# Performance work log

Measured on AMD Instinct MI355X. Metric: run time of the kernel, lower is better.

Reference implementation:

```python
import jax, jax.numpy as jnp
import numpy as np

# Static config (matches init_kwargs / link_info)
E = 8            # ep_size * num_local_experts
C = 1024         # expert capacity
D_IN = 4096      # in_features (d_ff)
D_OUT = 1024     # out_features (d_model)
B, S = 2, 2048   # inputs_shape = (B, S, D_OUT); tokens = B*S = 4096


def setup_inputs() -> dict:
    key = jax.random.key(0)
    ks = jax.random.split(key, 5)
    inputs = jax.random.normal(ks[0], (E * C + B * S, D_IN), dtype=jnp.float32)
    expert_w = jax.random.normal(ks[1], (E, D_IN, D_OUT), dtype=jnp.float32) * 0.02
    expert_b = jnp.zeros((E, D_OUT), dtype=jnp.float32)
    residual_w = jax.random.normal(ks[2], (D_IN, D_OUT), dtype=jnp.float32) * 0.02
    residual_b = jnp.zeros((D_OUT,), dtype=jnp.float32)
    combine_weights = jax.random.uniform(ks[3], (B * S, E, C), dtype=jnp.float32)
    residual_weight = jax.random.uniform(ks[4], (B, S, 2), dtype=jnp.float32)
    return {
        "inputs": inputs,
        "expert_w": expert_w,
        "expert_b": expert_b,
        "residual_w": residual_w,
        "residual_b": residual_b,
        "combine_weights": combine_weights,
        "residual_weight": residual_weight,
    }


def reference(inputs, expert_w, expert_b, residual_w, residual_b,
              combine_weights, residual_weight):
    # front_output: dispatched tokens [E, C, D_IN]
    front = inputs[: E * C].reshape(E, C, D_IN)
    # behind experts: per-expert second FFN linear -> [E, C, D_OUT]
    expert_out = jnp.einsum("ecd,edm->ecm", front, expert_w) + expert_b[:, None, :]
    # AllToAll over the expert-parallel group is identity for a single group.
    # combine: un-dispatch tokens, weighted scatter-gather 'sec,ecm->sm'
    combined = jnp.einsum("sec,ecm->sm", combine_weights, expert_out)
    output = combined.reshape(B, S, D_OUT)
    # residual MLP second linear on the tail slice of inputs
    resid_inter = inputs[E * C :].reshape(B, S, D_IN)
    resid_out = jnp.einsum("bsd,dm->bsm", resid_inter, residual_w) + residual_b
    # blend: output * w0 + residual * w1
    return output * residual_weight[..., 0:1] + resid_out * residual_weight[..., 1:]
```

## Files before the change

### kernel.cpp

```cpp
#include <hip/hip_runtime.h>
#include <hip/hip_bf16.h>

typedef __bf16 bf16_t;
typedef __bf16 bf16x8 __attribute__((ext_vector_type(8)));
typedef float f32x4 __attribute__((ext_vector_type(4)));

#define DEVI static __device__ __forceinline__

static constexpr int E_ = 8, C_ = 1024, DIN = 4096, DOUT = 1024, TOK = 4096;
static constexpr int BM = 128, BN = 128, BK = 64;
static constexpr int NT = 512;

static constexpr size_t WS_WT  = 0;
static constexpr size_t WS_RWT = WS_WT  + (size_t)E_ * DOUT * DIN * 2;
static constexpr size_t WS_EOT = WS_RWT + (size_t)DOUT * DIN * 2;

DEVI int swz(int row, int col) {
    return (col & ~63) | ((col & 56) ^ ((row & 7) << 3)) | (col & 7);
}

__global__ __launch_bounds__(256)
void transpose_cast_kernel(const float* __restrict__ expert_w,
                           const float* __restrict__ residual_w,
                           bf16_t* __restrict__ wt, bf16_t* __restrict__ rwt)
{
    __shared__ float tile[32][33];
    const int z = blockIdx.z;
    const float* src;
    bf16_t* dst;
    if (z < 8) { src = expert_w + (size_t)z * DIN * DOUT; dst = wt + (size_t)z * DOUT * DIN; }
    else       { src = residual_w;                         dst = rwt; }
    const int c0 = blockIdx.x * 32;
    const int r0 = blockIdx.y * 32;
    const int tx = threadIdx.x, ty = threadIdx.y;
#pragma unroll
    for (int k = 0; k < 4; ++k)
        tile[ty + 8 * k][tx] = src[(size_t)(r0 + ty + 8 * k) * DOUT + c0 + tx];
    __syncthreads();
#pragma unroll
    for (int k = 0; k < 4; ++k) {
        const int row = c0 + ty + 8 * k;
        const int col = r0 + tx;
        dst[(size_t)row * DIN + swz(row, col)] = (bf16_t)tile[tx][ty + 8 * k];
    }
}

template<int NELEM>
DEVI void stage_bf16(bf16_t* lds, const bf16_t* g, int ld, int tid)
{
    constexpr int PER_WAVE = NELEM / 8;
    constexpr int NI = PER_WAVE / 512;
    const int w = tid >> 6, l = tid & 63;
#pragma unroll
    for (int i = 0; i < NI; ++i) {
        const int eoff = w * PER_WAVE + i * 512 + l * 8;
        const int r = eoff >> 6, c = eoff & 63;
        const bf16_t* gp = g + (size_t)r * ld + c;
        bf16_t* lp = lds + w * PER_WAVE + i * 512;
        __builtin_amdgcn_global_load_lds(
            (const __attribute__((address_space(1))) void*)gp,
            (__attribute__((address_space(3))) void*)lp, 16, 0, 0);
    }
}

template<int NELEM>
DEVI void stage_f32(bf16_t* lds, const float* g, int ld, int tid)
{
    constexpr int NI = NELEM / (NT * 8);
#pragma unroll
    for (int i = 0; i < NI; ++i) {
        const int eoff = i * NT * 8 + tid * 8;
        const int r = eoff >> 6, c = eoff & 63;
        const float* gp = g + (size_t)r * ld + c;
        f32x4 v0 = *(const f32x4*)(gp);
        f32x4 v1 = *(const f32x4*)(gp + 4);
        bf16x8 h;
        h[0] = (bf16_t)v0[0]; h[1] = (bf16_t)v0[1];
        h[2] = (bf16_t)v0[2]; h[3] = (bf16_t)v0[3];
        h[4] = (bf16_t)v1[0]; h[5] = (bf16_t)v1[1];
        h[6] = (bf16_t)v1[2]; h[7] = (bf16_t)v1[3];
        const int cs = (c & 56) ^ ((r & 7) << 3);
        *(bf16x8*)(lds + r * 64 + cs) = h;
    }
}

__global__ __launch_bounds__(NT, 4)
void expert_gemm(const bf16_t* __restrict__ WT, const float* __restrict__ inputs,
                 bf16_t* __restrict__ EOT, const float* __restrict__ expert_b)
{
    __shared__ bf16_t As[BM * BK];
    __shared__ bf16_t Bs[BN * BK];
    const int tid = threadIdx.x;

    int id = blockIdx.x + 8 * (blockIdx.y + 8 * blockIdx.z);
    id = (id & 7) * 64 + (id >> 3);
    const int bx = id & 7, by = (id >> 3) & 7, e = id >> 6;

    const int brow = by * BM;
    const int bcol = bx * BN;
    const bf16_t* A = WT + (size_t)e * DOUT * DIN + (size_t)brow * DIN;
    const float*  B = inputs + (size_t)e * C_ * DIN + (size_t)bcol * DIN;

    const int w = tid >> 6, l = tid & 63;
    const int wr = (w >> 1) * 32, wc = (w & 1) * 64;
    const int lr = l & 15, lk = l >> 4, sw = (l & 7) << 3;

    f32x4 acc[2][4] = {};

    for (int k0 = 0; k0 < DIN; k0 += BK) {
        stage_bf16<BM * BK>(As, A + k0, DIN, tid);
        stage_f32<BN * BK>(Bs, B + k0, DIN, tid);
        __syncthreads();
#pragma unroll
        for (int kk = 0; kk < 2; ++kk) {
            const int cs = (kk * 32 + lk * 8) ^ sw;
            bf16x8 a[2], b[4];
#pragma unroll
            for (int m = 0; m < 2; ++m)
                a[m] = *(const bf16x8*)(&As[(wr + m * 16 + lr) * BK + cs]);
#pragma unroll
            for (int n = 0; n < 4; ++n)
                b[n] = *(const bf16x8*)(&Bs[(wc + n * 16 + lr) * BK + cs]);
#pragma unroll
            for (int m = 0; m < 2; ++m)
#pragma unroll
                for (int n = 0; n < 4; ++n)
                    acc[m][n] = __builtin_amdgcn_mfma_f32_16x16x32_bf16(a[m], b[n], acc[m][n], 0, 0, 0);
        }
        __syncthreads();
    }

#pragma unroll
    for (int m = 0; m < 2; ++m) {
#pragma unroll
        for (int n = 0; n < 4; ++n) {
            const int col = bcol + wc + n * 16 + lr;
#pragma unroll
            for (int j = 0; j < 4; ++j) {
                const int row = brow + wr + m * 16 + lk * 4 + j;
                const int ec = e * C_ + col;
                EOT[(size_t)row * (E_ * C_) + swz(row, ec)] =
                    (bf16_t)(acc[m][n][j] + expert_b[e * DOUT + row]);
            }
        }
    }
}

__global__ __launch_bounds__(NT, 4)
void combine_gemm(const float* __restrict__ cw, const bf16_t* __restrict__ EOT,
                  const float* __restrict__ xtail, const bf16_t* __restrict__ RWT,
                  const float* __restrict__ residual_b, const float* __restrict__ rw,
                  float* __restrict__ out)
{
    __shared__ bf16_t As[BM * BK];
    __shared__ bf16_t Bs[BN * BK];
    const int tid = threadIdx.x;

    int id = blockIdx.x + 8 * (blockIdx.y + 32 * blockIdx.z);
    id = (id & 7) * 96 + (id >> 3);
    const int bx = id & 7, by = (id >> 3) & 31, z = id >> 8;

    const int brow = by * BM;
    const int bcol = bx * BN;

    const float* A;
    const bf16_t* B;
    int ld;
    if (z == 0)      { A = cw + (size_t)brow * 8192;        B = EOT + (size_t)bcol * 8192;        ld = 8192; }
    else if (z == 1) { A = cw + (size_t)brow * 8192 + 4096; B = EOT + (size_t)bcol * 8192 + 4096; ld = 8192; }
    else             { A = xtail + (size_t)brow * 4096;     B = RWT + (size_t)bcol * 4096;        ld = 4096; }

    const int w = tid >> 6, l = tid & 63;
    const int wr = (w >> 1) * 32, wc = (w & 1) * 64;
    const int lr = l & 15, lk = l >> 4, sw = (l & 7) << 3;

    f32x4 acc[2][4] = {};

    for (int k0 = 0; k0 < 4096; k0 += BK) {
        stage_f32<BM * BK>(As, A + k0, ld, tid);
        stage_bf16<BN * BK>(Bs, B + k0, ld, tid);
        __syncthreads();
#pragma unroll
        for (int kk = 0; kk < 2; ++kk) {
            const int cs = (kk * 32 + lk * 8) ^ sw;
            bf16x8 a[2], b[4];
#pragma unroll
            for (int m = 0; m < 2; ++m)
                a[m] = *(const bf16x8*)(&As[(wr + m * 16 + lr) * BK + cs]);
#pragma unroll
            for (int n = 0; n < 4; ++n)
                b[n] = *(const bf16x8*)(&Bs[(wc + n * 16 + lr) * BK + cs]);
#pragma unroll
            for (int m = 0; m < 2; ++m)
#pragma unroll
                for (int n = 0; n < 4; ++n)
                    acc[m][n] = __builtin_amdgcn_mfma_f32_16x16x32_bf16(a[m], b[n], acc[m][n], 0, 0, 0);
        }
        __syncthreads();
    }

#pragma unroll
    for (int m = 0; m < 2; ++m) {
#pragma unroll
        for (int n = 0; n < 4; ++n) {
            const int col = bcol + wc + n * 16 + lr;
#pragma unroll
            for (int j = 0; j < 4; ++j) {
                const int row = brow + wr + m * 16 + lk * 4 + j;
                float v = acc[m][n][j];
                if (z == 2) v += residual_b[col];
                const float scale = rw[2 * row + (z == 2 ? 1 : 0)];
                atomicAdd(&out[(size_t)row * DOUT + col], scale * v);
            }
        }
    }
}

extern "C" void kernel_launch(void* const* d_in, const int* in_sizes, int n_in,
                              void* d_out, int out_size, void* d_ws, size_t ws_size,
                              hipStream_t stream)
{
    const float* inputs     = (const float*)d_in[0];
    const float* expert_w   = (const float*)d_in[1];
    const float* expert_b   = (const float*)d_in[2];
    const float* residual_w = (const float*)d_in[3];
    const float* residual_b = (const float*)d_in[4];
    const float* combine_w  = (const float*)d_in[5];
    const float* resid_wt   = (const float*)d_in[6];
    float* out = (float*)d_out;
    char* ws = (char*)d_ws;

    bf16_t* WT  = (bf16_t*)(ws + WS_WT);
    bf16_t* RWT = (bf16_t*)(ws + WS_RWT);
    bf16_t* EOT = (bf16_t*)(ws + WS_EOT);

    hipMemsetAsync(d_out, 0, (size_t)out_size * sizeof(float), stream);

    transpose_cast_kernel<<<dim3(32, 128, 9), dim3(32, 8), 0, stream>>>(
        expert_w, residual_w, WT, RWT);

    expert_gemm<<<dim3(C_ / BN, DOUT / BM, E_), NT, 0, stream>>>(
        WT, inputs, EOT, expert_b);

    combine_gemm<<<dim3(DOUT / BN, TOK / BM, 3), NT, 0, stream>>>(
        combine_w, EOT, inputs + (size_t)E_ * C_ * DIN, RWT,
        residual_b, resid_wt, out);
}
```

Measured before the change: 328.6 us.

## Double-buffer LDS tiles and prefetch next K-slice during MFMA in both GEMMs

Both GEMM kernels now use two LDS buffers per operand. The next K tile's bf16 operand is issued via global_load_lds, and its fp32 operand is loaded into registers before the current tile's MFMAs run. The fp32 data is then converted and written to the alternate buffer after compute, so only one barrier is needed per iteration. This aims to hide global memory latency behind matrix math. The cost is doubled LDS use (64KB per block), which may reduce the 4-blocks-per-CU occupancy, plus extra register pressure.

```diff
diff --git a/kernel.cpp b/kernel.cpp
--- a/kernel.cpp
+++ b/kernel.cpp
@@ -64,23 +64,34 @@
 }
 
 template<int NELEM>
-DEVI void stage_f32(bf16_t* lds, const float* g, int ld, int tid)
+DEVI void load_f32(f32x4* r, const float* __restrict__ g, int ld, int tid)
 {
     constexpr int NI = NELEM / (NT * 8);
 #pragma unroll
     for (int i = 0; i < NI; ++i) {
         const int eoff = i * NT * 8 + tid * 8;
-        const int r = eoff >> 6, c = eoff & 63;
-        const float* gp = g + (size_t)r * ld + c;
-        f32x4 v0 = *(const f32x4*)(gp);
-        f32x4 v1 = *(const f32x4*)(gp + 4);
+        const int rr = eoff >> 6, c = eoff & 63;
+        const float* gp = g + (size_t)rr * ld + c;
+        r[2 * i]     = *(const f32x4*)(gp);
+        r[2 * i + 1] = *(const f32x4*)(gp + 4);
+    }
+}
+
+template<int NELEM>
+DEVI void write_f32(bf16_t* lds, const f32x4* r, int tid)
+{
+    constexpr int NI = NELEM / (NT * 8);
+#pragma unroll
+    for (int i = 0; i < NI; ++i) {
+        const int eoff = i * NT * 8 + tid * 8;
+        const int rr = eoff >> 6, c = eoff & 63;
         bf16x8 h;
-        h[0] = (bf16_t)v0[0]; h[1] = (bf16_t)v0[1];
-        h[2] = (bf16_t)v0[2]; h[3] = (bf16_t)v0[3];
-        h[4] = (bf16_t)v1[0]; h[5] = (bf16_t)v1[1];
-        h[6] = (bf16_t)v1[2]; h[7] = (bf16_t)v1[3];
-        const int cs = (c & 56) ^ ((r & 7) << 3);
-        *(bf16x8*)(lds + r * 64 + cs) = h;
+        h[0] = (bf16_t)r[2 * i][0]; h[1] = (bf16_t)r[2 * i][1];
+        h[2] = (bf16_t)r[2 * i][2]; h[3] = (bf16_t)r[2 * i][3];
+        h[4] = (bf16_t)r[2 * i + 1][0]; h[5] = (bf16_t)r[2 * i + 1][1];
+        h[6] = (bf16_t)r[2 * i + 1][2]; h[7] = (bf16_t)r[2 * i + 1][3];
+        const int cs = (c & 56) ^ ((rr & 7) << 3);
+        *(bf16x8*)(lds + rr * 64 + cs) = h;
     }
 }
 
@@ -88,8 +99,8 @@
 void expert_gemm(const bf16_t* __restrict__ WT, const float* __restrict__ inputs,
                  bf16_t* __restrict__ EOT, const float* __restrict__ expert_b)
 {
-    __shared__ bf16_t As[BM * BK];
-    __shared__ bf16_t Bs[BN * BK];
+    __shared__ bf16_t As[2][BM * BK];
+    __shared__ bf16_t Bs[2][BN * BK];
     const int tid = threadIdx.x;
 
     int id = blockIdx.x + 8 * (blockIdx.y + 8 * blockIdx.z);
@@ -106,28 +117,39 @@
     const int lr = l & 15, lk = l >> 4, sw = (l & 7) << 3;
 
     f32x4 acc[2][4] = {};
-
+    f32x4 r[4];
+
+    stage_bf16<BM * BK>(As[0], A, DIN, tid);
+    load_f32<BN * BK>(r, B, DIN, tid);
+    write_f32<BN * BK>(Bs[0], r, tid);
+    __syncthreads();
+
+    int cur = 0;
     for (int k0 = 0; k0 < DIN; k0 += BK) {
-        stage_bf16<BM * BK>(As, A + k0, DIN, tid);
-        stage_f32<BN * BK>(Bs, B + k0, DIN, tid);
-        __syncthreads();
+        const bool more = (k0 + BK < DIN);
+        if (more) {
+            stage_bf16<BM * BK>(As[cur ^ 1], A + k0 + BK, DIN, tid);
+            load_f32<BN * BK>(r, B + k0 + BK, DIN, tid);
+        }
 #pragma unroll
         for (int kk = 0; kk < 2; ++kk) {
             const int cs = (kk * 32 + lk * 8) ^ sw;
             bf16x8 a[2], b[4];
 #pragma unroll
             for (int m = 0; m < 2; ++m)
-                a[m] = *(const bf16x8*)(&As[(wr + m * 16 + lr) * BK + cs]);
+                a[m] = *(const bf16x8*)(&As[cur][(wr + m * 16 + lr) * BK + cs]);
 #pragma unroll
             for (int n = 0; n < 4; ++n)
-                b[n] = *(const bf16x8*)(&Bs[(wc + n * 16 + lr) * BK + cs]);
+                b[n] = *(const bf16x8*)(&Bs[cur][(wc + n * 16 + lr) * BK + cs]);
 #pragma unroll
             for (int m = 0; m < 2; ++m)
 #pragma unroll
                 for (int n = 0; n < 4; ++n)
                     acc[m][n] = __builtin_amdgcn_mfma_f32_16x16x32_bf16(a[m], b[n], acc[m][n], 0, 0, 0);
         }
+        if (more) write_f32<BN * BK>(Bs[cur ^ 1], r, tid);
         __syncthreads();
+        cur ^= 1;
     }
 
 #pragma unroll
@@ -152,8 +174,8 @@
                   const float* __restrict__ residual_b, const float* __restrict__ rw,
                   float* __restrict__ out)
 {
-    __shared__ bf16_t As[BM * BK];
-    __shared__ bf16_t Bs[BN * BK];
+    __shared__ bf16_t As[2][BM * BK];
+    __shared__ bf16_t Bs[2][BN * BK];
     const int tid = threadIdx.x;
 
     int id = blockIdx.x + 8 * (blockIdx.y + 32 * blockIdx.z);
@@ -175,28 +197,39 @@
     const int lr = l & 15, lk = l >> 4, sw = (l & 7) << 3;
 
     f32x4 acc[2][4] = {};
-
+    f32x4 r[4];
+
+    stage_bf16<BN * BK>(Bs[0], B, ld, tid);
+    load_f32<BM * BK>(r, A, ld, tid);
+    write_f32<BM * BK>(As[0], r, tid);
+    __syncthreads();
+
+    int cur = 0;
     for (int k0 = 0; k0 < 4096; k0 += BK) {
-        stage_f32<BM * BK>(As, A + k0, ld, tid);
-        stage_bf16<BN * BK>(Bs, B + k0, ld, tid);
-        __syncthreads();
+        const bool more = (k0 + BK < 4096);
+        if (more) {
+            stage_bf16<BN * BK>(Bs[cur ^ 1], B + k0 + BK, ld, tid);
+            load_f32<BM * BK>(r, A + k0 + BK, ld, tid);
+        }
 #pragma unroll
         for (int kk = 0; kk < 2; ++kk) {
             const int cs = (kk * 32 + lk * 8) ^ sw;
             bf16x8 a[2], b[4];
 #pragma unroll
             for (int m = 0; m < 2; ++m)
-                a[m] = *(const bf16x8*)(&As[(wr + m * 16 + lr) * BK + cs]);
+                a[m] = *(const bf16x8*)(&As[cur][(wr + m * 16 + lr) * BK + cs]);
 #pragma unroll
             for (int n = 0; n < 4; ++n)
-                b[n] = *(const bf16x8*)(&Bs[(wc + n * 16 + lr) * BK + cs]);
+                b[n] = *(const bf16x8*)(&Bs[cur][(wc + n * 16 + lr) * BK + cs]);
 #pragma unroll
             for (int m = 0; m < 2; ++m)
 #pragma unroll
                 for (int n = 0; n < 4; ++n)
                     acc[m][n] = __builtin_amdgcn_mfma_f32_16x16x32_bf16(a[m], b[n], acc[m][n], 0, 0, 0);
         }
+        if (more) write_f32<BM * BK>(As[cur ^ 1], r, tid);
         __syncthreads();
+        cur ^= 1;
     }
 
 #pragma unroll
```

After: 390.8 us. 18.9% more time.

## Load combine-GEMM A operand directly to registers, shrink block to four waves

Applied to the files above, without the earlier changes.

The combine GEMM stops staging the fp32 A tile through LDS. Each lane now loads its fp32 rows straight from global memory into registers and converts them to bf16 in place before the MFMA. The block drops to 256 threads with four waves, each owning a 64x64 output subtile with a 4x4 accumulator array. Only the bf16 B tile still goes through LDS. This removes the LDS writes, reads and bank traffic for A. In exchange each thread holds more registers, occupancy falls (launch bounds 256,3), and the direct global loads are less coalesced.

```diff
diff --git a/kernel.cpp b/kernel.cpp
--- a/kernel.cpp
+++ b/kernel.cpp
@@ -45,10 +45,10 @@
     }
 }
 
-template<int NELEM>
+template<int NELEM, int NW>
 DEVI void stage_bf16(bf16_t* lds, const bf16_t* g, int ld, int tid)
 {
-    constexpr int PER_WAVE = NELEM / 8;
+    constexpr int PER_WAVE = NELEM / NW;
     constexpr int NI = PER_WAVE / 512;
     const int w = tid >> 6, l = tid & 63;
 #pragma unroll
@@ -64,7 +64,7 @@
 }
 
 template<int NELEM>
-DEVI void stage_f32(bf16_t* lds, const float* g, int ld, int tid)
+DEVI void stage_f32(bf16_t* lds, const float* __restrict__ g, int ld, int tid)
 {
     constexpr int NI = NELEM / (NT * 8);
 #pragma unroll
@@ -108,7 +108,7 @@
     f32x4 acc[2][4] = {};
 
     for (int k0 = 0; k0 < DIN; k0 += BK) {
-        stage_bf16<BM * BK>(As, A + k0, DIN, tid);
+        stage_bf16<BM * BK, 8>(As, A + k0, DIN, tid);
         stage_f32<BN * BK>(Bs, B + k0, DIN, tid);
         __syncthreads();
 #pragma unroll
@@ -146,13 +146,12 @@
     }
 }
 
-__global__ __launch_bounds__(NT, 4)
+__global__ __launch_bounds__(256, 3)
 void combine_gemm(const float* __restrict__ cw, const bf16_t* __restrict__ EOT,
                   const float* __restrict__ xtail, const bf16_t* __restrict__ RWT,
                   const float* __restrict__ residual_b, const float* __restrict__ rw,
                   float* __restrict__ out)
 {
-    __shared__ bf16_t As[BM * BK];
     __shared__ bf16_t Bs[BN * BK];
     const int tid = threadIdx.x;
 
@@ -171,36 +170,51 @@
     else             { A = xtail + (size_t)brow * 4096;     B = RWT + (size_t)bcol * 4096;        ld = 4096; }
 
     const int w = tid >> 6, l = tid & 63;
-    const int wr = (w >> 1) * 32, wc = (w & 1) * 64;
+    const int wr = (w >> 1) * 64, wc = (w & 1) * 64;
     const int lr = l & 15, lk = l >> 4, sw = (l & 7) << 3;
 
-    f32x4 acc[2][4] = {};
+    const float* Alane = A + (size_t)(wr + lr) * ld + lk * 8;
+
+    f32x4 acc[4][4] = {};
 
     for (int k0 = 0; k0 < 4096; k0 += BK) {
-        stage_f32<BM * BK>(As, A + k0, ld, tid);
-        stage_bf16<BN * BK>(Bs, B + k0, ld, tid);
+        stage_bf16<BN * BK, 4>(Bs, B + k0, ld, tid);
+        f32x4 ar[4][2][2];
+#pragma unroll
+        for (int m = 0; m < 4; ++m) {
+            const float* ap = Alane + (size_t)m * 16 * ld + k0;
+#pragma unroll
+            for (int kk = 0; kk < 2; ++kk) {
+                ar[m][kk][0] = *(const f32x4*)(ap + kk * 32);
+                ar[m][kk][1] = *(const f32x4*)(ap + kk * 32 + 4);
+            }
+        }
         __syncthreads();
 #pragma unroll
         for (int kk = 0; kk < 2; ++kk) {
             const int cs = (kk * 32 + lk * 8) ^ sw;
-            bf16x8 a[2], b[4];
-#pragma unroll
-            for (int m = 0; m < 2; ++m)
-                a[m] = *(const bf16x8*)(&As[(wr + m * 16 + lr) * BK + cs]);
+            bf16x8 b[4];
 #pragma unroll
             for (int n = 0; n < 4; ++n)
                 b[n] = *(const bf16x8*)(&Bs[(wc + n * 16 + lr) * BK + cs]);
 #pragma unroll
-            for (int m = 0; m < 2; ++m)
+            for (int m = 0; m < 4; ++m) {
+                bf16x8 a;
+#pragma unroll
+                for (int j = 0; j < 4; ++j) {
+                    a[j]     = (bf16_t)ar[m][kk][0][j];
+                    a[j + 4] = (bf16_t)ar[m][kk][1][j];
+                }
 #pragma unroll
                 for (int n = 0; n < 4; ++n)
-                    acc[m][n] = __builtin_amdgcn_mfma_f32_16x16x32_bf16(a[m], b[n], acc[m][n], 0, 0, 0);
-        }
-        __syncthreads();
-    }
-
-#pragma unroll
-    for (int m = 0; m < 2; ++m) {
+                    acc[m][n] = __builtin_amdgcn_mfma_f32_16x16x32_bf16(a, b[n], acc[m][n], 0, 0, 0);
+            }
+        }
+        __syncthreads();
+    }
+
+#pragma unroll
+    for (int m = 0; m < 4; ++m) {
 #pragma unroll
         for (int n = 0; n < 4; ++n) {
             const int col = bcol + wc + n * 16 + lr;
@@ -242,7 +256,7 @@
     expert_gemm<<<dim3(C_ / BN, DOUT / BM, E_), NT, 0, stream>>>(
         WT, inputs, EOT, expert_b);
 
-    combine_gemm<<<dim3(DOUT / BN, TOK / BM, 3), NT, 0, stream>>>(
+    combine_gemm<<<dim3(8, 32, 3), 256, 0, stream>>>(
         combine_w, EOT, inputs + (size_t)E_ * C_ * DIN, RWT,
         residual_b, resid_wt, out);
 }
```

New measurement: 580.8 us. 76.7% more time.
